# Performance work log

Hardware: AMD Instinct MI355X
Metric: run time of the kernel (lower is better)

Reference implementation:

```python
import jax, jax.numpy as jnp
import numpy as np
from jax import lax

KERNEL = 9
STRIDE = 1
PAD = 4


def setup_inputs() -> dict:
    key = jax.random.key(0)
    kx, kk = jax.random.split(key)
    X = jax.random.normal(kx, (32, 64, 256, 256), dtype=jnp.float32)
    # single shared kernel, applied to every channel (Parameter(1,1,k,k))
    K = jax.random.normal(kk, (1, 1, KERNEL, KERNEL), dtype=jnp.float32)
    return {"X": X, "K": K}


def reference(X, K):
    # Depthwise cross-correlation with one shared kxk kernel:
    # out[b,c,i,j] = sum_{u,v} X_pad[b,c,i*s+u, j*s+v] * K[0,0,u,v]
    B, C, H, W = X.shape
    Xr = X.reshape(B * C, 1, H, W)  # treat each channel as its own sample
    out = lax.conv_general_dilated(
        Xr, K,
        window_strides=(STRIDE, STRIDE),
        padding=[(PAD, PAD), (PAD, PAD)],
        dimension_numbers=("NCHW", "OIHW", "NCHW"),
    )
    return out.reshape(B, C, out.shape[2], out.shape[3])
```

## Files before the change

kernel.cpp:

```cpp
#include <hip/hip_runtime.h>


#define CONV_H 256
#define CONV_W 256
#define TILE 64
#define HALO 4
#define LDS_DIM 72
#define NPLANES 2048

__global__ __launch_bounds__(256)
void conv9x9_kernel(const float* __restrict__ X,
                    const float* __restrict__ K,
                    float* __restrict__ out)
{
    __shared__ float lds[LDS_DIM * LDS_DIM];

    const int tid   = threadIdx.x;
    const int bid   = blockIdx.x;
    const int plane = bid >> 4;
    const int tile  = bid & 15;
    const int tile_y = (tile >> 2) << 6;
    const int tile_x = (tile & 3) << 6;

    const float* Xp = X + (size_t)plane * (CONV_H * CONV_W);

    float kw[81];
#pragma unroll
    for (int i = 0; i < 81; ++i) kw[i] = K[i];

    for (int s = tid; s < LDS_DIM * (LDS_DIM / 4); s += 256) {
        int row  = s / (LDS_DIM / 4);
        int colv = s - row * (LDS_DIM / 4);
        int gy = tile_y - HALO + row;
        int gx = tile_x - HALO + colv * 4;
        float4 v = make_float4(0.f, 0.f, 0.f, 0.f);
        if ((unsigned)gy < CONV_H && (unsigned)gx < CONV_W) {
            v = *reinterpret_cast<const float4*>(Xp + gy * CONV_W + gx);
        }
        *reinterpret_cast<float4*>(&lds[row * LDS_DIM + colv * 4]) = v;
    }
    __syncthreads();

    const int tx  = tid & 15;
    const int ty  = tid >> 4;
    const int ox0 = tx << 2;
    const int oy0 = ty << 2;

    float acc[4][4] = {{0.f}};

#pragma unroll
    for (int r = 0; r < 12; ++r) {
        float rowv[12];
        const float* lp = &lds[(oy0 + r) * LDS_DIM + ox0];
        *reinterpret_cast<float4*>(&rowv[0]) = *reinterpret_cast<const float4*>(lp);
        *reinterpret_cast<float4*>(&rowv[4]) = *reinterpret_cast<const float4*>(lp + 4);
        *reinterpret_cast<float4*>(&rowv[8]) = *reinterpret_cast<const float4*>(lp + 8);
#pragma unroll
        for (int i = 0; i < 4; ++i) {
            const int u = r - i;
            if (u >= 0 && u < 9) {
#pragma unroll
                for (int v = 0; v < 9; ++v) {
                    const float w = kw[u * 9 + v];
#pragma unroll
                    for (int j = 0; j < 4; ++j)
                        acc[i][j] = fmaf(rowv[v + j], w, acc[i][j]);
                }
            }
        }
    }

    float* Op = out + (size_t)plane * (CONV_H * CONV_W)
                    + (size_t)(tile_y + oy0) * CONV_W + (tile_x + ox0);
#pragma unroll
    for (int i = 0; i < 4; ++i) {
        float4 v = make_float4(acc[i][0], acc[i][1], acc[i][2], acc[i][3]);
        *reinterpret_cast<float4*>(Op + i * CONV_W) = v;
    }
}

extern "C" void kernel_launch(void* const* d_in, const int* in_sizes, int n_in,
                              void* d_out, int out_size, void* d_ws, size_t ws_size,
                              hipStream_t stream) {
    const float* X = (const float*)d_in[0];
    const float* K = (const float*)d_in[1];
    float* out = (float*)d_out;

    const int nblocks = NPLANES * 16;
    conv9x9_kernel<<<nblocks, 256, 0, stream>>>(X, K, out);
}
```

Baseline: 937.9 us.

## Replace LDS tiling with direct global row loads and per-plane blocks

```diff
diff --git a/kernel.cpp b/kernel.cpp
--- a/kernel.cpp
+++ b/kernel.cpp
@@ -3,9 +3,6 @@
 
 #define CONV_H 256
 #define CONV_W 256
-#define TILE 64
-#define HALO 4
-#define LDS_DIM 72
 #define NPLANES 2048
 
 __global__ __launch_bounds__(256)
@@ -13,69 +10,70 @@
                     const float* __restrict__ K,
                     float* __restrict__ out)
 {
-    __shared__ float lds[LDS_DIM * LDS_DIM];
+    const int tid  = threadIdx.x;
+    const int lane = tid & 63;
+    const int wv   = tid >> 6;
+    const int plane = blockIdx.x;
 
-    const int tid   = threadIdx.x;
-    const int bid   = blockIdx.x;
-    const int plane = bid >> 4;
-    const int tile  = bid & 15;
-    const int tile_y = (tile >> 2) << 6;
-    const int tile_x = (tile & 3) << 6;
+    const int x0 = lane << 2;
+    const int y0 = __builtin_amdgcn_readfirstlane(wv << 6);
 
-    const float* Xp = X + (size_t)plane * (CONV_H * CONV_W);
+    const float* __restrict__ Xp = X + (size_t)plane * (CONV_H * CONV_W);
+    float* __restrict__ Op       = out + (size_t)plane * (CONV_H * CONV_W);
 
     float kw[81];
 #pragma unroll
     for (int i = 0; i < 81; ++i) kw[i] = K[i];
 
-    for (int s = tid; s < LDS_DIM * (LDS_DIM / 4); s += 256) {
-        int row  = s / (LDS_DIM / 4);
-        int colv = s - row * (LDS_DIM / 4);
-        int gy = tile_y - HALO + row;
-        int gx = tile_x - HALO + colv * 4;
-        float4 v = make_float4(0.f, 0.f, 0.f, 0.f);
-        if ((unsigned)gy < CONV_H && (unsigned)gx < CONV_W) {
-            v = *reinterpret_cast<const float4*>(Xp + gy * CONV_W + gx);
-        }
-        *reinterpret_cast<float4*>(&lds[row * LDS_DIM + colv * 4]) = v;
-    }
-    __syncthreads();
+    const int   offA = (x0 == 0)   ? 0   : (x0 - 4);
+    const int   offC = (x0 == 252) ? 248 : (x0 + 4);
+    const float mL   = (x0 == 0)   ? 0.f : 1.f;
+    const float mR   = (x0 == 252) ? 0.f : 1.f;
 
-    const int tx  = tid & 15;
-    const int ty  = tid >> 4;
-    const int ox0 = tx << 2;
-    const int oy0 = ty << 2;
-
-    float acc[4][4] = {{0.f}};
+    for (int c = 0; c < 16; ++c) {
+        const int oy = y0 + (c << 2);
+        float acc[4][4] = {{0.f}};
 
 #pragma unroll
-    for (int r = 0; r < 12; ++r) {
-        float rowv[12];
-        const float* lp = &lds[(oy0 + r) * LDS_DIM + ox0];
-        *reinterpret_cast<float4*>(&rowv[0]) = *reinterpret_cast<const float4*>(lp);
-        *reinterpret_cast<float4*>(&rowv[4]) = *reinterpret_cast<const float4*>(lp + 4);
-        *reinterpret_cast<float4*>(&rowv[8]) = *reinterpret_cast<const float4*>(lp + 8);
+        for (int r = 0; r < 12; ++r) {
+            const int gy = oy - 4 + r;
+            float rowv[12];
+            if ((unsigned)gy < CONV_H) {
+                const float* rb = Xp + gy * CONV_W;
+                const float4 a = *reinterpret_cast<const float4*>(rb + offA);
+                const float4 b = *reinterpret_cast<const float4*>(rb + x0);
+                const float4 d = *reinterpret_cast<const float4*>(rb + offC);
+                rowv[0] = a.x * mL; rowv[1] = a.y * mL;
+                rowv[2] = a.z * mL; rowv[3] = a.w * mL;
+                rowv[4] = b.x; rowv[5] = b.y; rowv[6] = b.z; rowv[7] = b.w;
+                rowv[8] = d.x * mR; rowv[9] = d.y * mR;
+                rowv[10] = d.z * mR; rowv[11] = d.w * mR;
+            } else {
 #pragma unroll
-        for (int i = 0; i < 4; ++i) {
-            const int u = r - i;
-            if (u >= 0 && u < 9) {
+                for (int j = 0; j < 12; ++j) rowv[j] = 0.f;
+            }
+
 #pragma unroll
-                for (int v = 0; v < 9; ++v) {
-                    const float w = kw[u * 9 + v];
+            for (int i = 0; i < 4; ++i) {
+                const int u = r - i;
+                if (u >= 0 && u < 9) {
 #pragma unroll
-                    for (int j = 0; j < 4; ++j)
-                        acc[i][j] = fmaf(rowv[v + j], w, acc[i][j]);
+                    for (int v = 0; v < 9; ++v) {
+                        const float w = kw[u * 9 + v];
+#pragma unroll
+                        for (int j = 0; j < 4; ++j)
+                            acc[i][j] = fmaf(rowv[v + j], w, acc[i][j]);
+                    }
                 }
             }
         }
-    }
 
-    float* Op = out + (size_t)plane * (CONV_H * CONV_W)
-                    + (size_t)(tile_y + oy0) * CONV_W + (tile_x + ox0);
+        float* op = Op + (size_t)oy * CONV_W + x0;
 #pragma unroll
-    for (int i = 0; i < 4; ++i) {
-        float4 v = make_float4(acc[i][0], acc[i][1], acc[i][2], acc[i][3]);
-        *reinterpret_cast<float4*>(Op + i * CONV_W) = v;
+        for (int i = 0; i < 4; ++i) {
+            *reinterpret_cast<float4*>(op + i * CONV_W) =
+                make_float4(acc[i][0], acc[i][1], acc[i][2], acc[i][3]);
+        }
     }
 }
 
@@ -86,6 +84,5 @@
     const float* K = (const float*)d_in[1];
     float* out = (float*)d_out;
 
-    const int nblocks = NPLANES * 16;
-    conv9x9_kernel<<<nblocks, 256, 0, stream>>>(X, K, out);
+    conv9x9_kernel<<<NPLANES, 256, 0, stream>>>(X, K, out);
 }
```

Measured after the change: 1.611 ms. 1.72x slower.
